# Optimization experiments

Measured on AMD Instinct MI355X. Metric: run time of the kernel, lower is better.

Reference implementation:

```python
import jax, jax.numpy as jnp
import numpy as np

B, T, H, OUT = 2048, 512, 256, 512


def setup_inputs() -> dict:
    key = jax.random.key(0)
    ks = jax.random.split(key, 7)
    s = 1.0 / np.sqrt(H)  # PyTorch LSTM/Linear default uniform bound
    u = lambda k, shape: jax.random.uniform(k, shape, jnp.float32, -s, s)
    return {
        "x": jax.random.normal(ks[0], (B, T, 1), jnp.float32),
        "W_ih": u(ks[1], (4 * H, 1)),
        "W_hh": u(ks[2], (4 * H, H)),
        "b_ih": u(ks[3], (4 * H,)),
        "b_hh": u(ks[4], (4 * H,)),
        "W_lin": u(ks[5], (OUT, H)),
        "b_lin": u(ks[6], (OUT,)),
    }


def reference(x, W_ih, W_hh, b_ih, b_hh, W_lin, b_lin):
    # x: [B, T, 1]. Precompute input projection for all timesteps: [B, T, 4H]
    b, t = x.shape[0], x.shape[1]
    h = W_hh.shape[1]
    x_proj = jnp.einsum('bti,gi->btg', x, W_ih) + (b_ih + b_hh)

    def step(carry, xt):  # xt: [B, 4H]
        h_prev, c_prev = carry
        gates = xt + h_prev @ W_hh.T  # [B, 4H]
        i, f, g, o = jnp.split(gates, 4, axis=-1)  # PyTorch gate order i,f,g,o
        i = jax.nn.sigmoid(i)
        f = jax.nn.sigmoid(f)
        g = jnp.tanh(g)
        o = jax.nn.sigmoid(o)
        c = f * c_prev + i * g
        h_new = o * jnp.tanh(c)
        return (h_new, c), None

    init = (jnp.zeros((b, h), x.dtype), jnp.zeros((b, h), x.dtype))
    xs = jnp.swapaxes(x_proj, 0, 1)  # [T, B, 4H]
    (h_last, _), _ = jax.lax.scan(step, init, xs)

    # Dropout(0.2) is identity in eval mode; last-step slice == final hidden state.
    return h_last @ W_lin.T + b_lin  # [B, OUT]
```

## Files before the change

### kernel.cpp

```cpp
#include <hip/hip_runtime.h>
#include <cstdint>

typedef _Float16 half8 __attribute__((ext_vector_type(8)));
typedef float floatx4 __attribute__((ext_vector_type(4)));
typedef unsigned long long u64;
typedef unsigned int u32;
typedef unsigned short u16;

#define NB 2048
#define NT 512
#define NH 256
#define NOUT 512
#define BROWS 8

#define LOG2E 1.4426950408889634f
#define TWOL  2.8853900817779268f

__device__ __forceinline__ float fexp2(float x){ return __builtin_amdgcn_exp2f(x); }
__device__ __forceinline__ float frcp(float x){ return __builtin_amdgcn_rcpf(x); }

__device__ __forceinline__ floatx4 mfma16(half8 a, half8 b, floatx4 c) {
    return __builtin_amdgcn_mfma_f32_16x16x32_f16(a, b, c, 0, 0, 0);
}

__global__ void prep_kernel(const float* __restrict__ x, const float* __restrict__ Whh,
                            const float* __restrict__ Wlin, _Float16* __restrict__ Wpack,
                            _Float16* __restrict__ WlinPack, float* __restrict__ xT)
{
    const int b = blockIdx.x;
    if (b < 1024) {
        __shared__ float tile[32][33];
        const int tx = threadIdx.x & 31, ty = threadIdx.x >> 5;
        const int t0 = (b & 15) * 32;
        const int b0 = (b >> 4) * 32;
        #pragma unroll
        for (int i = 0; i < 4; i++)
            tile[ty + 8 * i][tx] = x[(size_t)(b0 + ty + 8 * i) * NT + t0 + tx];
        __syncthreads();
        #pragma unroll
        for (int i = 0; i < 4; i++)
            xT[(size_t)(t0 + ty + 8 * i) * NB + b0 + tx] = tile[tx][ty + 8 * i];
    } else {
        const int i = (b - 1024) * 256 + threadIdx.x;
        const int stride = 256 * 256;
        for (int k = i; k < 1024 * 256; k += stride) Wpack[k]    = (_Float16)Whh[k];
        for (int k = i; k < 512 * 256;  k += stride) WlinPack[k] = (_Float16)Wlin[k];
    }
}

template<int FUSED>
__global__ __launch_bounds__(512, 1)
void lstm_kernel(const float* __restrict__ xT, const float* __restrict__ Wih,
                 const float* __restrict__ bih, const float* __restrict__ bhh,
                 const _Float16* __restrict__ Wpack, const _Float16* __restrict__ WlinPack,
                 const float* __restrict__ blin, float* __restrict__ outp,
                 u16* __restrict__ hlast)
{
    __shared__ __align__(16) u16 wlds[16][4096];
    __shared__ __align__(16) u16 hlds[2][4096];
    __shared__ float2 bwlds[1024];

    const int tid  = threadIdx.x;
    const int lane = tid & 63;
    const int wv   = tid >> 6;
    const int l15  = lane & 15;
    const int l4   = lane >> 4;
    const int r0   = blockIdx.x * BROWS;
    const int u0   = wv * 32;

    for (int g = tid; g < 1024; g += 512) bwlds[g] = make_float2(bih[g] + bhh[g], Wih[g]);
    for (int i = tid; i < 2048; i += 512) ((u64*)hlds[0])[i] = 0;

    for (int ch = tid; ch < 8192; ch += 512) {
        const int tl = ch >> 9;
        const int cc = ch & 511;
        const int row = cc >> 5;
        const int kch = cc & 31;
        const int G  = 768 + (tl >> 1) * 32 + (tl & 1) * 16 + row;
        half8 v = *(const half8*)(Wpack + (size_t)G * NH + kch * 8);
        *(half8*)(&wlds[tl][kch * 128 + row * 8]) = v;
    }

    half8 wreg[2][3][8];
    #pragma unroll
    for (int ug = 0; ug < 2; ug++)
        #pragma unroll
        for (int q = 0; q < 3; q++) {
            const int G = q * 256 + u0 + ug * 16 + l15;
            #pragma unroll
            for (int kc = 0; kc < 8; kc++)
                wreg[ug][q][kc] = *(const half8*)(Wpack + (size_t)G * NH + kc * 32 + l4 * 8);
        }

    float cst[8];
    #pragma unroll
    for (int i = 0; i < 8; i++) cst[i] = 0.f;

    __syncthreads();

    for (int t = 0; t < NT; t++) {
        const u16* hsrc = hlds[t & 1];
        u16*       hdst = hlds[(t + 1) & 1];
        const floatx4 xv = *(const floatx4*)(xT + (size_t)t * NB + r0 + (l4 & 1) * 4);

        #pragma unroll
        for (int ug = 0; ug < 2; ug++) {
            floatx4 acc[4];
            #pragma unroll
            for (int q = 0; q < 4; q++)
                acc[q] = (floatx4){0.f, 0.f, 0.f, 0.f};

            __builtin_amdgcn_s_setprio(1);
            #pragma unroll
            for (int half_ = 0; half_ < 2; half_++) {
                half8 a[4];
                #pragma unroll
                for (int k2 = 0; k2 < 4; k2++) {
                    const int kc = half_ * 4 + k2;
                    a[k2] = *(const half8*)(hsrc + (kc * 4 + l4) * 128 + l15 * 8);
                }
                #pragma unroll
                for (int k2 = 0; k2 < 4; k2++) {
                    const int kc = half_ * 4 + k2;
                    const half8 b3 = *(const half8*)(&wlds[wv * 2 + ug][(kc * 4 + l4) * 128 + l15 * 8]);
                    acc[0] = mfma16(a[k2], wreg[ug][0][kc], acc[0]);
                    acc[1] = mfma16(a[k2], wreg[ug][1][kc], acc[1]);
                    acc[2] = mfma16(a[k2], wreg[ug][2][kc], acc[2]);
                    acc[3] = mfma16(a[k2], b3,              acc[3]);
                }
            }
            __builtin_amdgcn_s_setprio(0);

            if (l4 < 2) {
                float2 bw[4];
                #pragma unroll
                for (int q = 0; q < 4; q++) bw[q] = bwlds[q * 256 + u0 + ug * 16 + l15];

                #pragma unroll
                for (int j = 0; j < 4; j++) {
                    const float pi = acc[0][j] + bw[0].x + xv[j] * bw[0].y;
                    const float pf = acc[1][j] + bw[1].x + xv[j] * bw[1].y;
                    const float pg = acc[2][j] + bw[2].x + xv[j] * bw[2].y;
                    const float po = acc[3][j] + bw[3].x + xv[j] * bw[3].y;
                    const float ei = fexp2(-LOG2E * pi);
                    const float ef = fexp2(-LOG2E * pf);
                    const float eo = fexp2(-LOG2E * po);
                    const float eg = fexp2(TWOL * pg);
                    const float f  = frcp(1.f + ef);
                    const float ig = (eg - 1.f) * frcp((eg + 1.f) * (1.f + ei));
                    const float cc = f * cst[ug * 4 + j] + ig;
                    cst[ug * 4 + j] = cc;
                    const float ec = fexp2(fminf(TWOL * cc, 126.f));
                    const float h  = (ec - 1.f) * frcp((ec + 1.f) * (1.f + eo));
                    const int row  = l4 * 4 + j;
                    const int unit = u0 + ug * 16 + l15;
                    const u16 hb = __builtin_bit_cast(u16, (_Float16)h);
                    const u32 ob = (u16)__shfl_xor((int)hb, 1, 64);
                    if ((l15 & 1) == 0) {
                        const u32 packed = (u32)hb | (ob << 16);
                        const int idx = (unit >> 3) * 128 + row * 8 + (unit & 6);
                        *(u32*)(&hdst[idx]) = packed;
                    }
                }
            }
        }
        __syncthreads();
    }

    if constexpr (FUSED) {
        const u16* hT = hlds[0];
        half8 af[8];
        #pragma unroll
        for (int kc = 0; kc < 8; kc++)
            af[kc] = *(const half8*)(hT + (kc * 4 + l4) * 128 + l15 * 8);
        const int o0 = wv * 64;
        #pragma unroll
        for (int nt = 0; nt < 4; nt++) {
            const int col = o0 + nt * 16 + l15;
            floatx4 accL = (floatx4){0.f, 0.f, 0.f, 0.f};
            #pragma unroll
            for (int kc = 0; kc < 8; kc++) {
                const half8 b = *(const half8*)(WlinPack + (size_t)col * NH + kc * 32 + l4 * 8);
                accL = mfma16(af[kc], b, accL);
            }
            const float bb = blin[col];
            if (l4 < 2) {
                #pragma unroll
                for (int j = 0; j < 4; j++)
                    outp[(size_t)(r0 + l4 * 4 + j) * NOUT + col] = accL[j] + bb;
            }
        }
    } else {
        for (int i = tid; i < BROWS * 256; i += 512) {
            const int row = i >> 8, unit = i & 255;
            hlast[(size_t)(r0 + row) * NH + unit] =
                hlds[0][(unit >> 3) * 128 + row * 8 + (unit & 7)];
        }
    }
}

__global__ __launch_bounds__(256, 2)
void linear_kernel(const u16* __restrict__ hlast_u, const _Float16* __restrict__ WlinPack,
                   const float* __restrict__ blin, float* __restrict__ out)
{
    const int tid = threadIdx.x;
    const int lane = tid & 63;
    const int wv = tid >> 6;
    const int mi = wv >> 1, ni = wv & 1;
    const int l15 = lane & 15, l4 = lane >> 4;
    const int r0 = (blockIdx.x >> 3) * 32;
    const int o0 = (blockIdx.x & 7) * 64;
    const _Float16* hl = (const _Float16*)hlast_u;
    const int arow = r0 + mi * 16 + l15;

    half8 a[8];
    #pragma unroll
    for (int kc = 0; kc < 8; kc++)
        a[kc] = *(const half8*)(hl + (size_t)arow * NH + kc * 32 + l4 * 8);

    #pragma unroll
    for (int nt = 0; nt < 2; nt++) {
        const int col = o0 + ni * 32 + nt * 16 + l15;
        floatx4 acc = (floatx4){0.f, 0.f, 0.f, 0.f};
        #pragma unroll
        for (int kc = 0; kc < 8; kc++) {
            const half8 b = *(const half8*)(WlinPack + (size_t)col * NH + kc * 32 + l4 * 8);
            acc = mfma16(a[kc], b, acc);
        }
        const float bb = blin[col];
        #pragma unroll
        for (int j = 0; j < 4; j++) {
            const int row = r0 + mi * 16 + l4 * 4 + j;
            out[(size_t)row * NOUT + col] = acc[j] + bb;
        }
    }
}

extern "C" void kernel_launch(void* const* d_in, const int* in_sizes, int n_in,
                              void* d_out, int out_size, void* d_ws, size_t ws_size,
                              hipStream_t stream)
{
    const float* x    = (const float*)d_in[0];
    const float* Wih  = (const float*)d_in[1];
    const float* Whh  = (const float*)d_in[2];
    const float* bih  = (const float*)d_in[3];
    const float* bhh  = (const float*)d_in[4];
    const float* Wlin = (const float*)d_in[5];
    const float* blin = (const float*)d_in[6];

    char* ws = (char*)d_ws;
    _Float16* Wpack    = (_Float16*)(ws);
    _Float16* WlinPack = (_Float16*)(ws + (512 << 10));

    const size_t need_fused = (768 << 10) + (size_t)NT * NB * 4;
    const bool fused = ws_size >= need_fused;

    if (fused) {
        float* xT = (float*)(ws + (768 << 10));
        prep_kernel<<<1280, 256, 0, stream>>>(x, Whh, Wlin, Wpack, WlinPack, xT);
        lstm_kernel<1><<<256, 512, 0, stream>>>(xT, Wih, bih, bhh, Wpack,
                                                WlinPack, blin, (float*)d_out, nullptr);
    } else {
        u16*   hlast = (u16*)(ws + (768 << 10));
        float* xT    = (float*)d_out;
        prep_kernel<<<1280, 256, 0, stream>>>(x, Whh, Wlin, Wpack, WlinPack, xT);
        lstm_kernel<0><<<256, 512, 0, stream>>>(xT, Wih, bih, bhh, Wpack,
                                                WlinPack, blin, nullptr, hlast);
        linear_kernel<<<512, 256, 0, stream>>>(hlast, WlinPack, blin, (float*)d_out);
    }
}
```

Baseline: 1.331 ms.

## Fill all MFMA rows with 16 batch rows per block and prescale gate weights

Each block now handles 16 batch rows instead of 8. All four lane groups of the 16x16 MFMA tile carry real rows and all lanes run the activation stage, and the grid is halved to 128 blocks. The exp2 scale factors (-log2e, 2log2e) are folded into the fp16 recurrent weights, biases and input weights, so the per-step gate multiplies disappear. The time loop is unrolled by two with separate ping-pong h buffers, which removes the buffer index arithmetic. Because the recurrence is latency-bound, the halved grid may leave half the CUs idle without shortening each step, and prescaling before the fp16 cast slightly changes rounding.

```diff
diff --git a/kernel.cpp b/kernel.cpp
--- a/kernel.cpp
+++ b/kernel.cpp
@@ -11,7 +11,6 @@
 #define NT 512
 #define NH 256
 #define NOUT 512
-#define BROWS 8
 
 #define LOG2E 1.4426950408889634f
 #define TWOL  2.8853900817779268f
@@ -43,7 +42,11 @@
     } else {
         const int i = (b - 1024) * 256 + threadIdx.x;
         const int stride = 256 * 256;
-        for (int k = i; k < 1024 * 256; k += stride) Wpack[k]    = (_Float16)Whh[k];
+        for (int k = i; k < 1024 * 256; k += stride) {
+            const int row = k >> 8;
+            const float s = (row >= 512 && row < 768) ? TWOL : -LOG2E;
+            Wpack[k] = (_Float16)(s * Whh[k]);
+        }
         for (int k = i; k < 512 * 256;  k += stride) WlinPack[k] = (_Float16)Wlin[k];
     }
 }
@@ -57,7 +60,8 @@
                  u16* __restrict__ hlast)
 {
     __shared__ __align__(16) u16 wlds[16][4096];
-    __shared__ __align__(16) u16 hlds[2][4096];
+    __shared__ __align__(16) u16 hA[4096];
+    __shared__ __align__(16) u16 hB[4096];
     __shared__ float2 bwlds[1024];
 
     const int tid  = threadIdx.x;
@@ -65,11 +69,14 @@
     const int wv   = tid >> 6;
     const int l15  = lane & 15;
     const int l4   = lane >> 4;
-    const int r0   = blockIdx.x * BROWS;
+    const int r0   = blockIdx.x * 16;
     const int u0   = wv * 32;
 
-    for (int g = tid; g < 1024; g += 512) bwlds[g] = make_float2(bih[g] + bhh[g], Wih[g]);
-    for (int i = tid; i < 2048; i += 512) ((u64*)hlds[0])[i] = 0;
+    for (int g = tid; g < 1024; g += 512) {
+        const float s = (g >= 512 && g < 768) ? TWOL : -LOG2E;
+        bwlds[g] = make_float2(s * (bih[g] + bhh[g]), s * Wih[g]);
+    }
+    for (int i = tid; i < 1024; i += 512) ((u64*)hA)[i] = 0;
 
     for (int ch = tid; ch < 8192; ch += 512) {
         const int tl = ch >> 9;
@@ -98,10 +105,8 @@
 
     __syncthreads();
 
-    for (int t = 0; t < NT; t++) {
-        const u16* hsrc = hlds[t & 1];
-        u16*       hdst = hlds[(t + 1) & 1];
-        const floatx4 xv = *(const floatx4*)(xT + (size_t)t * NB + r0 + (l4 & 1) * 4);
+    auto step = [&](int t, const u16* hsrc, u16* hdst) {
+        const floatx4 xv = *(const floatx4*)(xT + (size_t)t * NB + r0 + l4 * 4);
 
         #pragma unroll
         for (int ug = 0; ug < 2; ug++) {
@@ -131,48 +136,50 @@
             }
             __builtin_amdgcn_s_setprio(0);
 
-            if (l4 < 2) {
-                float2 bw[4];
-                #pragma unroll
-                for (int q = 0; q < 4; q++) bw[q] = bwlds[q * 256 + u0 + ug * 16 + l15];
-
-                #pragma unroll
-                for (int j = 0; j < 4; j++) {
-                    const float pi = acc[0][j] + bw[0].x + xv[j] * bw[0].y;
-                    const float pf = acc[1][j] + bw[1].x + xv[j] * bw[1].y;
-                    const float pg = acc[2][j] + bw[2].x + xv[j] * bw[2].y;
-                    const float po = acc[3][j] + bw[3].x + xv[j] * bw[3].y;
-                    const float ei = fexp2(-LOG2E * pi);
-                    const float ef = fexp2(-LOG2E * pf);
-                    const float eo = fexp2(-LOG2E * po);
-                    const float eg = fexp2(TWOL * pg);
-                    const float f  = frcp(1.f + ef);
-                    const float ig = (eg - 1.f) * frcp((eg + 1.f) * (1.f + ei));
-                    const float cc = f * cst[ug * 4 + j] + ig;
-                    cst[ug * 4 + j] = cc;
-                    const float ec = fexp2(fminf(TWOL * cc, 126.f));
-                    const float h  = (ec - 1.f) * frcp((ec + 1.f) * (1.f + eo));
-                    const int row  = l4 * 4 + j;
-                    const int unit = u0 + ug * 16 + l15;
-                    const u16 hb = __builtin_bit_cast(u16, (_Float16)h);
-                    const u32 ob = (u16)__shfl_xor((int)hb, 1, 64);
-                    if ((l15 & 1) == 0) {
-                        const u32 packed = (u32)hb | (ob << 16);
-                        const int idx = (unit >> 3) * 128 + row * 8 + (unit & 6);
-                        *(u32*)(&hdst[idx]) = packed;
-                    }
+            float2 bw[4];
+            #pragma unroll
+            for (int q = 0; q < 4; q++) bw[q] = bwlds[q * 256 + u0 + ug * 16 + l15];
+
+            #pragma unroll
+            for (int j = 0; j < 4; j++) {
+                const float pi = acc[0][j] + bw[0].x + xv[j] * bw[0].y;
+                const float pf = acc[1][j] + bw[1].x + xv[j] * bw[1].y;
+                const float pg = acc[2][j] + bw[2].x + xv[j] * bw[2].y;
+                const float po = acc[3][j] + bw[3].x + xv[j] * bw[3].y;
+                const float ei = fexp2(pi);
+                const float ef = fexp2(pf);
+                const float eo = fexp2(po);
+                const float eg = fexp2(pg);
+                const float f  = frcp(1.f + ef);
+                const float ig = (eg - 1.f) * frcp((eg + 1.f) * (1.f + ei));
+                const float cc = f * cst[ug * 4 + j] + ig;
+                cst[ug * 4 + j] = cc;
+                const float ec = fexp2(fminf(TWOL * cc, 126.f));
+                const float h  = (ec - 1.f) * frcp((ec + 1.f) * (1.f + eo));
+                const int row  = l4 * 4 + j;
+                const int unit = u0 + ug * 16 + l15;
+                const u16 hb = __builtin_bit_cast(u16, (_Float16)h);
+                const u32 ob = (u16)__shfl_xor((int)hb, 1, 64);
+                if ((l15 & 1) == 0) {
+                    const u32 packed = (u32)hb | (ob << 16);
+                    const int idx = (unit >> 3) * 128 + row * 8 + (unit & 6);
+                    *(u32*)(&hdst[idx]) = packed;
                 }
             }
         }
         __syncthreads();
+    };
+
+    for (int t = 0; t < NT; t += 2) {
+        step(t,     hA, hB);
+        step(t + 1, hB, hA);
     }
 
     if constexpr (FUSED) {
-        const u16* hT = hlds[0];
         half8 af[8];
         #pragma unroll
         for (int kc = 0; kc < 8; kc++)
-            af[kc] = *(const half8*)(hT + (kc * 4 + l4) * 128 + l15 * 8);
+            af[kc] = *(const half8*)(hA + (kc * 4 + l4) * 128 + l15 * 8);
         const int o0 = wv * 64;
         #pragma unroll
         for (int nt = 0; nt < 4; nt++) {
@@ -184,17 +191,15 @@
                 accL = mfma16(af[kc], b, accL);
             }
             const float bb = blin[col];
-            if (l4 < 2) {
-                #pragma unroll
-                for (int j = 0; j < 4; j++)
-                    outp[(size_t)(r0 + l4 * 4 + j) * NOUT + col] = accL[j] + bb;
-            }
+            #pragma unroll
+            for (int j = 0; j < 4; j++)
+                outp[(size_t)(r0 + l4 * 4 + j) * NOUT + col] = accL[j] + bb;
         }
     } else {
-        for (int i = tid; i < BROWS * 256; i += 512) {
+        for (int i = tid; i < 4096; i += 512) {
             const int row = i >> 8, unit = i & 255;
             hlast[(size_t)(r0 + row) * NH + unit] =
-                hlds[0][(unit >> 3) * 128 + row * 8 + (unit & 7)];
+                hA[(unit >> 3) * 128 + row * 8 + (unit & 7)];
         }
     }
 }
@@ -258,13 +263,13 @@
     if (fused) {
         float* xT = (float*)(ws + (768 << 10));
         prep_kernel<<<1280, 256, 0, stream>>>(x, Whh, Wlin, Wpack, WlinPack, xT);
-        lstm_kernel<1><<<256, 512, 0, stream>>>(xT, Wih, bih, bhh, Wpack,
+        lstm_kernel<1><<<128, 512, 0, stream>>>(xT, Wih, bih, bhh, Wpack,
                                                 WlinPack, blin, (float*)d_out, nullptr);
     } else {
         u16*   hlast = (u16*)(ws + (768 << 10));
         float* xT    = (float*)d_out;
         prep_kernel<<<1280, 256, 0, stream>>>(x, Whh, Wlin, Wpack, WlinPack, xT);
-        lstm_kernel<0><<<256, 512, 0, stream>>>(xT, Wih, bih, bhh, Wpack,
+        lstm_kernel<0><<<128, 512, 0, stream>>>(xT, Wih, bih, bhh, Wpack,
                                                 WlinPack, blin, nullptr, hlast);
         linear_kernel<<<512, 256, 0, stream>>>(hlast, WlinPack, blin, (float*)d_out);
     }
```

Result: faster. 1.188 ms (-10.7%).
